# Optimization experiments

Measured on AMD Instinct MI355X. Metric: run time of the kernel, lower is better.

The kernel has to match this reference:

```python
import jax, jax.numpy as jnp
import numpy as np

ENC_IN = 512
D_MODEL = 1024
EMB_DIM = 32
IN_DIM = D_MODEL + EMB_DIM  # 1056
BATCH = 64


def setup_inputs() -> dict:
    key = jax.random.key(0)
    ks = jax.random.split(key, 12)
    s = 0.02
    return {
        "x": jax.random.normal(ks[0], (BATCH, ENC_IN, D_MODEL), dtype=jnp.float32),
        "emb": jax.random.normal(ks[1], (ENC_IN, EMB_DIM), dtype=jnp.float32) * s,
        # weights stored [in, out] (transposed vs torch Linear, same math)
        "w1": jax.random.normal(ks[2], (IN_DIM, IN_DIM), dtype=jnp.float32) * s,
        "b1": jnp.zeros((IN_DIM,), dtype=jnp.float32),
        "wq": jax.random.normal(ks[3], (IN_DIM, IN_DIM), dtype=jnp.float32) * s,
        "bq": jnp.zeros((IN_DIM,), dtype=jnp.float32),
        "wk": jax.random.normal(ks[4], (IN_DIM, IN_DIM), dtype=jnp.float32) * s,
        "bk": jnp.zeros((IN_DIM,), dtype=jnp.float32),
        "wv": jax.random.normal(ks[5], (IN_DIM, IN_DIM), dtype=jnp.float32) * s,
        "bv": jnp.zeros((IN_DIM,), dtype=jnp.float32),
        "w2": jax.random.normal(ks[6], (IN_DIM, D_MODEL), dtype=jnp.float32) * s,
        "b2": jnp.zeros((D_MODEL,), dtype=jnp.float32),
    }


def reference(x, emb, w1, b1, wq, bq, wk, bk, wv, bv, w2, b2):
    B = x.shape[0]
    # variable embedding: same for every batch element -> broadcast concat
    e = jnp.broadcast_to(emb[None, :, :], (B, ENC_IN, EMB_DIM))
    h = jnp.concatenate([x, e], axis=2)                      # [B, S, IN_DIM]
    h = jax.nn.leaky_relu(h @ w1 + b1, negative_slope=0.2)   # l1
    # hand-rolled self-attention: no scaling, softmax over last dim
    q = h @ wq + bq
    k = h @ wk + bk
    v = h @ wv + bv
    energy = jnp.einsum("bsd,btd->bst", q, k)                # [B, S, S]
    attn = jax.nn.softmax(energy, axis=-1)
    out = jnp.einsum("bst,btd->bsd", attn, v)                # [B, S, IN_DIM]
    return out @ w2 + b2                                     # [B, S, D_MODEL]
```

## Files before the change

### kernel.cpp

```cpp
#include <hip/hip_runtime.h>
#include <hip/hip_bf16.h>
#include <cstdint>

typedef __hip_bfloat16 bf16;
typedef __attribute__((ext_vector_type(8))) short short8;
typedef __attribute__((ext_vector_type(4))) float f32x4;

__device__ __forceinline__ void gload16(const bf16* g, bf16* l) {
    __builtin_amdgcn_global_load_lds(
        (__attribute__((address_space(1))) void*)g,
        (__attribute__((address_space(3))) void*)l, 16, 0, 0);
}
#define VMC(n) asm volatile("s_waitcnt vmcnt(" #n ")" ::: "memory")
__device__ __forceinline__ void bar() {
    asm volatile("" ::: "memory");
    __builtin_amdgcn_s_barrier();
    asm volatile("" ::: "memory");
}

__device__ __forceinline__ void stage_half(const bf16* __restrict__ G, int ld,
                                           int row0, int k0, bf16* lregion,
                                           int w, int lrow, int lslot)
{
    const bf16* s0 = G + (long long)(row0 + w * 8 + lrow) * ld + (k0 + lslot * 8);
    gload16(s0, lregion + (w * 64) * 8);
    gload16(s0 + (long long)64 * ld, lregion + (512 + w * 64) * 8);
}

#define LOAD_AI(dst, i_, mh, P) do { \
    _Pragma("unroll") for (int ks_ = 0; ks_ < 2; ++ks_) \
      dst[i_][ks_] = *(const short8*)((P) + ((mh) * 64 + (i_) * 16 + l15) * 64 \
                                         + (((ks_ * 4 + lq) ^ l7) * 8)); } while (0)
#define LOAD_B(nh, dst) do { _Pragma("unroll") for (int j_ = 0; j_ < 2; ++j_) { \
    _Pragma("unroll") for (int ks_ = 0; ks_ < 2; ++ks_) \
      dst[j_][ks_] = *(const short8*)(pb + (bhr + (nh) * 32 + j_ * 16 + l15) * 64 \
                                         + (((ks_ * 4 + lq) ^ l7) * 8)); } } while (0)
#define DO_Q(mh, nh, AF, BF) do { \
    __builtin_amdgcn_s_setprio(1); \
    _Pragma("unroll") for (int i_ = 0; i_ < 4; ++i_) \
      _Pragma("unroll") for (int j_ = 0; j_ < 2; ++j_) \
        _Pragma("unroll") for (int ks_ = 0; ks_ < 2; ++ks_) \
          acc[mh][nh][i_][j_] = __builtin_amdgcn_mfma_f32_16x16x32_bf16( \
              AF[i_][ks_], BF[j_][ks_], acc[mh][nh][i_][j_], 0, 0, 0); \
    __builtin_amdgcn_s_setprio(0); \
} while (0)

template<int OUT_BF16, int ACT, int BIASMODE, int ROUTE>
__global__ __launch_bounds__(512, 2)
void gemm256(const bf16* __restrict__ Abase, const bf16* __restrict__ Bbase,
             void* __restrict__ Cbase, const float* __restrict__ bias,
             int K, int lda, int ldb, int ldc, int nwrite,
             long long sA, long long sB, long long sC, long long segStride)
{
    __shared__ bf16 lds[2][2][2][8192];

    const int gx = gridDim.x, gy = gridDim.y;
    const int nwg = gx * gy * gridDim.z;
    const int lin = blockIdx.x + gx * (blockIdx.y + gy * blockIdx.z);
    const int qch = nwg >> 3, rch = nwg & 7;
    const int xcd = lin & 7, pos = lin >> 3;
    const int nl = (xcd < rch ? xcd * (qch + 1)
                              : rch * (qch + 1) + (xcd - rch) * qch) + pos;
    const int bz = nl / (gx * gy);
    const int rem = nl - bz * (gx * gy);
    const int by = rem / gx;
    const int bx = rem - by * gx;

    const int tid = threadIdx.x;
    const int wid = tid >> 6, lane = tid & 63;
    const int wm = wid >> 2, wn = wid & 3;
    const int l15 = lane & 15, l7 = lane & 7, lq = lane >> 4;
    const int lrow = lane >> 3, lslot = l7 ^ lrow;
    const int bhr = (wn & 1) * 64;

    const bf16* A = Abase + (long long)bz * sA;
    const bf16* B = Bbase + (long long)bz * sB;
    const int brow = by * 256, bcol = bx * 256;

    f32x4 acc[2][2][4][2] = {};
    short8 aFe[4][2], aFo[4][2], bF0[2][2], bF1[2][2];

    const int nt = K >> 6;

    stage_half(B, ldb, bcol,       0,  &lds[0][1][0][0], wid, lrow, lslot);
    stage_half(B, ldb, bcol + 128, 0,  &lds[0][1][1][0], wid, lrow, lslot);
    stage_half(A, lda, brow,       0,  &lds[0][0][0][0], wid, lrow, lslot);
    stage_half(A, lda, brow + 128, 0,  &lds[0][0][1][0], wid, lrow, lslot);
    stage_half(B, ldb, bcol,       64, &lds[1][1][0][0], wid, lrow, lslot);
    stage_half(B, ldb, bcol + 128, 64, &lds[1][1][1][0], wid, lrow, lslot);
    VMC(4);
    bar();

    for (int t = 0; t < nt; ++t) {
        const int b = t & 1;
        const bf16* pa = &lds[b][0][wm][0];
        const bf16* pb = &lds[b][1][wn >> 1][0];
        bf16* oA = &lds[b ^ 1][0][0][0];
        bf16* cB = &lds[b][1][0][0];
        const int t1 = (t + 1 == nt) ? 0 : t + 1;
        const int t2 = (t + 2 >= nt) ? t + 2 - nt : t + 2;
        const int k1 = t1 << 6, k2 = t2 << 6;

        LOAD_B(0, bF0);
        LOAD_AI(aFe, 0, 0, pa); LOAD_AI(aFe, 1, 0, pa);
        LOAD_AI(aFe, 2, 0, pa); LOAD_AI(aFe, 3, 0, pa);
        LOAD_B(1, bF1);
        stage_half(A, lda, brow, k1, oA, wid, lrow, lslot);
        bar();
        DO_Q(0, 0, aFe, bF0);
        bar();

        LOAD_AI(aFo, 0, 1, pa); LOAD_AI(aFo, 1, 1, pa);
        stage_half(A, lda, brow + 128, k1, oA + 8192, wid, lrow, lslot);
        bar();
        DO_Q(0, 1, aFe, bF1);
        bar();

        LOAD_AI(aFo, 2, 1, pa); LOAD_AI(aFo, 3, 1, pa);
        stage_half(B, ldb, bcol, k2, cB, wid, lrow, lslot);
        bar();
        DO_Q(1, 1, aFo, bF1);
        bar();

        stage_half(B, ldb, bcol + 128, k2, cB + 8192, wid, lrow, lslot);
        bar();
        DO_Q(1, 0, aFo, bF0);
        VMC(4);
        bar();
    }
    VMC(0);

    const long long cofs0 = (long long)bz * sC;
    #pragma unroll
    for (int mh = 0; mh < 2; ++mh)
      #pragma unroll
      for (int nh = 0; nh < 2; ++nh)
        #pragma unroll
        for (int i = 0; i < 4; ++i)
          #pragma unroll
          for (int j = 0; j < 2; ++j) {
              const int gc = bcol + wn * 64 + nh * 32 + j * 16 + l15;
              const bool wr = gc < nwrite;
              const int row0 = brow + wm * 128 + mh * 64 + i * 16 + lq * 4;
              if (wr) {
                  float bvv = 0.0f;
                  if (BIASMODE == 1) bvv = bias[gc];
                  if (BIASMODE == 3) bvv = bias[(long long)bz * 512 + gc];
                  if (ROUTE == 2 && gc < 1152) {
                      const int b_ = row0 >> 9, s_ = row0 & 511;
                      bf16 t4[4];
                      #pragma unroll
                      for (int rr = 0; rr < 4; ++rr) {
                          float vv = acc[mh][nh][i][j][rr] + bvv;
                          t4[rr] = (bf16)vv;
                      }
                      *(ushort4*)&((bf16*)Cbase)[((long long)b_ * 1280 + gc) * 512 + s_]
                          = *(ushort4*)t4;
                  } else {
                      long long base; int lc, ld;
                      if (ROUTE == 2) { base = segStride; lc = gc - 1152; ld = 1088; }
                      else { base = cofs0; lc = gc; ld = ldc; }
                      #pragma unroll
                      for (int rr = 0; rr < 4; ++rr) {
                          float vv = acc[mh][nh][i][j][rr] + bvv;
                          if (ACT) vv = vv > 0.0f ? vv : 0.2f * vv;
                          const long long cidx = base + (long long)(row0 + rr) * ld + lc;
                          if (OUT_BF16) ((bf16*)Cbase)[cidx] = (bf16)vv;
                          else          ((float*)Cbase)[cidx] = vv;
                      }
                  }
              }
          }
}

__global__ void concat_cast_kernel(const float* __restrict__ x,
                                   const float* __restrict__ emb,
                                   bf16* __restrict__ out)
{
    const int m = blockIdx.x;
    const int s = m & 511;
    const float* xr = x + (long long)m * 1024;
    bf16* orow = out + (long long)m * 1088;
    for (int g = threadIdx.x; g < 272; g += 256) {
        const int c = g * 4;
        float4 v;
        if (c < 1024)      v = *(const float4*)&xr[c];
        else if (c < 1056) v = *(const float4*)&emb[s * 32 + (c - 1024)];
        else               v = make_float4(0.f, 0.f, 0.f, 0.f);
        bf16 t[4] = { (bf16)v.x, (bf16)v.y, (bf16)v.z, (bf16)v.w };
        *(ushort4*)&orow[c] = *(ushort4*)t;
    }
}

__global__ void wprep_kernel(const float* __restrict__ w1, const float* __restrict__ wv,
                             const float* __restrict__ w2, const float* __restrict__ wq,
                             const float* __restrict__ wk,
                             bf16* __restrict__ w1T, bf16* __restrict__ Bqv,
                             bf16* __restrict__ w2T, bf16* __restrict__ wqC,
                             bf16* __restrict__ wkC)
{
    const int z = blockIdx.z;
    const int tx = threadIdx.x, ty = threadIdx.y;
    if (z >= 3) {
        const float* src = (z == 3) ? wq : wk;
        bf16* dst = (z == 3) ? wqC : wkC;
        const int r = blockIdx.y * 32 + ty, c = blockIdx.x * 32 + tx;
        if (r < 1280 && c < 1088) {
            float v = (r < 1056 && c < 1056) ? src[(long long)r * 1056 + c] : 0.0f;
            dst[(long long)r * 1088 + c] = (bf16)v;
        }
        return;
    }
    const float* src; bf16* dst; int NIN, NP, srcld;
    switch (z) {
        case 0: src = w1; dst = w1T; NIN = 1056; NP = 1280; srcld = 1056; break;
        case 1: src = wv; dst = Bqv; NIN = 1056; NP = 1152; srcld = 1056; break;
        default: src = w2; dst = w2T; NIN = 1024; NP = 1024; srcld = 1024; break;
    }
    const int KIN = 1056, KP = 1088;
    const int k0 = blockIdx.x * 32, n0 = blockIdx.y * 32;
    if (n0 >= NP) return;
    __shared__ float t[32][33];
    const int kk = k0 + ty, nn = n0 + tx;
    t[ty][tx] = (kk < KIN && nn < NIN) ? src[(long long)kk * srcld + nn] : 0.0f;
    __syncthreads();
    const int ko = k0 + tx, no = n0 + ty;
    if (no < NP && ko < KP)
        dst[(long long)no * KP + ko] = (bf16)t[tx][ty];
}

__global__ void vtzero_kernel(bf16* __restrict__ vt)
{
    const long long i = ((long long)blockIdx.x * 256 + threadIdx.x) * 8;
    const int per_batch = 128 * 512;
    const int b = (int)(i / per_batch);
    const long long r = i - (long long)b * per_batch;
    ushort4 z4 = make_ushort4(0, 0, 0, 0);
    bf16* p = &vt[(long long)b * (1280LL * 512) + 1152LL * 512 + r];
    *(ushort4*)p = z4;
    *(ushort4*)(p + 4) = z4;
}

__global__ void uvec_kernel(const float* __restrict__ wk, const float* __restrict__ bq,
                            float* __restrict__ u)
{
    const int wid = threadIdx.x >> 6, lane = threadIdx.x & 63;
    const int e = blockIdx.x * 4 + wid;
    if (e >= 1088) return;
    float s = 0.0f;
    if (e < 1056) {
        for (int d = lane; d < 1056; d += 64)
            s += wk[(long long)e * 1056 + d] * bq[d];
    }
    #pragma unroll
    for (int sh = 32; sh > 0; sh >>= 1) s += __shfl_xor(s, sh);
    if (lane == 0) u[e] = s;
}

__global__ __launch_bounds__(256)
void cvec_kernel(const bf16* __restrict__ h, const float* __restrict__ u,
                 float* __restrict__ c)
{
    const int wid = threadIdx.x >> 6, lane = threadIdx.x & 63;
    const long long row = (long long)blockIdx.x * 4 + wid;
    const bf16* hr = h + row * 1088;
    float s = 0.0f;
    #pragma unroll
    for (int j = 0; j < 17; ++j)
        s += (float)hr[j * 64 + lane] * u[j * 64 + lane];
    #pragma unroll
    for (int sh = 32; sh > 0; sh >>= 1) s += __shfl_xor(s, sh);
    if (lane == 0) c[row] = s;
}

__global__ void biasprep_kernel(const float* __restrict__ b1, const float* __restrict__ bv,
                                const float* __restrict__ b2,
                                float* __restrict__ b1p, float* __restrict__ bqv2,
                                float* __restrict__ b2p)
{
    const int i = blockIdx.x * 256 + threadIdx.x;
    if (i < 1088) {
        b1p[i] = (i < 1056) ? b1[i] : 0.0f;
    } else if (i < 1088 + 2304) {
        const int j = i - 1088;
        bqv2[j] = (j < 1056) ? bv[j] : 0.0f;
    } else if (i < 1088 + 2304 + 1024) {
        b2p[i - (1088 + 2304)] = b2[i - (1088 + 2304)];
    }
}

__global__ __launch_bounds__(256)
void softmax_kernel(const float* __restrict__ e, bf16* __restrict__ p)
{
    const int wid = threadIdx.x >> 6, lane = threadIdx.x & 63;
    const long long row = (long long)blockIdx.x * 4 + wid;
    const float* er = e + row * 512;
    float v[8];
    float mx = -3.0e38f;
    #pragma unroll
    for (int j = 0; j < 8; ++j) { v[j] = er[j * 64 + lane]; mx = fmaxf(mx, v[j]); }
    #pragma unroll
    for (int s = 32; s > 0; s >>= 1) mx = fmaxf(mx, __shfl_xor(mx, s));
    float sum = 0.0f;
    #pragma unroll
    for (int j = 0; j < 8; ++j) { v[j] = __expf(v[j] - mx); sum += v[j]; }
    #pragma unroll
    for (int s = 32; s > 0; s >>= 1) sum += __shfl_xor(sum, s);
    const float inv = 1.0f / sum;
    bf16* pr = p + row * 512;
    #pragma unroll
    for (int j = 0; j < 8; ++j) pr[j * 64 + lane] = (bf16)(v[j] * inv);
}

extern "C" void kernel_launch(void* const* d_in, const int* in_sizes, int n_in,
                              void* d_out, int out_size, void* d_ws, size_t ws_size,
                              hipStream_t stream)
{
    const float* x   = (const float*)d_in[0];
    const float* emb = (const float*)d_in[1];
    const float* w1  = (const float*)d_in[2];
    const float* b1  = (const float*)d_in[3];
    const float* wq  = (const float*)d_in[4];
    const float* bq  = (const float*)d_in[5];
    const float* wk  = (const float*)d_in[6];
    const float* wv  = (const float*)d_in[8];
    const float* bv  = (const float*)d_in[9];
    const float* w2  = (const float*)d_in[10];
    const float* b2  = (const float*)d_in[11];
    float* out = (float*)d_out;

    const long long Mrows = 32768;
    const int KR = 1088;

    char* ws = (char*)d_ws;
    size_t off = 0;
    auto alloc = [&](size_t bytes) -> char* {
        char* p = ws + off;
        off += (bytes + 255) & ~(size_t)255;
        return p;
    };
    char* R1   = alloc((size_t)Mrows * KR * 2);
    char* Rh   = alloc((size_t)Mrows * KR * 2);
    char* Rq   = alloc((size_t)Mrows * KR * 2);
    bf16* vT   = (bf16*)alloc((size_t)64 * 1280 * 512 * 2);
    bf16* w1T  = (bf16*)alloc((size_t)1280 * KR * 2);
    bf16* Bqv  = (bf16*)alloc((size_t)2432 * KR * 2);
    bf16* w2T  = (bf16*)alloc((size_t)1024 * KR * 2);
    bf16* wqC  = (bf16*)alloc((size_t)1280 * KR * 2);
    bf16* wkC  = (bf16*)alloc((size_t)1280 * KR * 2);
    float* b1p  = (float*)alloc((size_t)1088 * 4);
    float* bqv2 = (float*)alloc((size_t)2304 * 4);
    float* b2p  = (float*)alloc((size_t)1024 * 4);
    float* uvec = (float*)alloc((size_t)1088 * 4);
    float* cvec = (float*)alloc((size_t)Mrows * 4);

    bf16*  hcat   = (bf16*)R1;
    float* energy = (float*)R1;
    bf16*  pv     = (bf16*)R1;
    bf16*  h      = (bf16*)Rh;
    bf16*  qbuf   = (bf16*)Rq;
    bf16*  attn   = (bf16*)Rq;

    concat_cast_kernel<<<32768, 256, 0, stream>>>(x, emb, hcat);
    wprep_kernel<<<dim3(34, 40, 5), dim3(32, 32), 0, stream>>>(
        w1, wv, w2, wq, wk, w1T, Bqv, w2T, wqC, wkC);
    uvec_kernel<<<272, 256, 0, stream>>>(wk, bq, uvec);
    biasprep_kernel<<<18, 256, 0, stream>>>(b1, bv, b2, b1p, bqv2, b2p);
    vtzero_kernel<<<2048, 256, 0, stream>>>(vT);

    gemm256<1, 0, 0, 0><<<dim3(5, 5, 1), 512, 0, stream>>>(
        wkC, wqC, Bqv + 1152LL * KR, nullptr,
        KR, KR, KR, KR, KR, 0, 0, 0, 0);
    gemm256<1, 1, 1, 0><<<dim3(5, 128, 1), 512, 0, stream>>>(
        hcat, w1T, h, b1p, KR, KR, KR, KR, KR, 0, 0, 0, 0);
    cvec_kernel<<<8192, 256, 0, stream>>>(h, uvec, cvec);
    gemm256<1, 0, 1, 2><<<dim3(9, 128, 1), 512, 0, stream>>>(
        h, Bqv, vT, bqv2, KR, KR, KR, 0, 2240, 0, 0, 0,
        (long long)(qbuf - vT));
    gemm256<0, 0, 3, 0><<<dim3(2, 2, 64), 512, 0, stream>>>(
        qbuf, h, energy, cvec, KR, KR, KR, 512, 512,
        512LL * KR, 512LL * KR, 512LL * 512, 0);
    softmax_kernel<<<8192, 256, 0, stream>>>(energy, attn);
    gemm256<1, 0, 0, 0><<<dim3(5, 2, 64), 512, 0, stream>>>(
        attn, vT, pv, nullptr, 512, 512, 512, KR, KR,
        512LL * 512, 1280LL * 512, 512LL * KR, 0);
    gemm256<0, 0, 1, 0><<<dim3(4, 128, 1), 512, 0, stream>>>(
        pv, w2T, out, b2p, KR, KR, KR, 1024, 1024, 0, 0, 0, 0);
}
```

Measured before the change: 600.7 us.

## Fold w2 into value projection to drop final output GEMM

Precomputes Wv·W2 as a combined weight (plus bv·W2 + b2 as a bias) so the V projection directly produces a 1024-wide v2 in transposed layout, and attention-times-v2 writes the final output. This removes the separate pv buffer and the final full-size projection GEMM, and also the vT padding-zero kernel. The cost is an extra small weight-product GEMM and a serial bias kernel, and a change in bf16 rounding order because the products are fused into one weight.

```diff
diff --git a/kernel.cpp b/kernel.cpp
--- a/kernel.cpp
+++ b/kernel.cpp
@@ -146,7 +146,7 @@
                   float bvv = 0.0f;
                   if (BIASMODE == 1) bvv = bias[gc];
                   if (BIASMODE == 3) bvv = bias[(long long)bz * 512 + gc];
-                  if (ROUTE == 2 && gc < 1152) {
+                  if (ROUTE == 2 && gc < 1024) {
                       const int b_ = row0 >> 9, s_ = row0 & 511;
                       bf16 t4[4];
                       #pragma unroll
@@ -154,11 +154,11 @@
                           float vv = acc[mh][nh][i][j][rr] + bvv;
                           t4[rr] = (bf16)vv;
                       }
-                      *(ushort4*)&((bf16*)Cbase)[((long long)b_ * 1280 + gc) * 512 + s_]
+                      *(ushort4*)&((bf16*)Cbase)[((long long)b_ * 1024 + gc) * 512 + s_]
                           = *(ushort4*)t4;
                   } else {
                       long long base; int lc, ld;
-                      if (ROUTE == 2) { base = segStride; lc = gc - 1152; ld = 1088; }
+                      if (ROUTE == 2) { base = segStride; lc = gc - 1024; ld = 1088; }
                       else { base = cofs0; lc = gc; ld = ldc; }
                       #pragma unroll
                       for (int rr = 0; rr < 4; ++rr) {
@@ -195,15 +195,15 @@
 __global__ void wprep_kernel(const float* __restrict__ w1, const float* __restrict__ wv,
                              const float* __restrict__ w2, const float* __restrict__ wq,
                              const float* __restrict__ wk,
-                             bf16* __restrict__ w1T, bf16* __restrict__ Bqv,
+                             bf16* __restrict__ w1T, bf16* __restrict__ wvC,
                              bf16* __restrict__ w2T, bf16* __restrict__ wqC,
                              bf16* __restrict__ wkC)
 {
     const int z = blockIdx.z;
     const int tx = threadIdx.x, ty = threadIdx.y;
-    if (z >= 3) {
-        const float* src = (z == 3) ? wq : wk;
-        bf16* dst = (z == 3) ? wqC : wkC;
+    if (z == 1 || z >= 3) {
+        const float* src = (z == 1) ? wv : (z == 3) ? wq : wk;
+        bf16* dst = (z == 1) ? wvC : (z == 3) ? wqC : wkC;
         const int r = blockIdx.y * 32 + ty, c = blockIdx.x * 32 + tx;
         if (r < 1280 && c < 1088) {
             float v = (r < 1056 && c < 1056) ? src[(long long)r * 1056 + c] : 0.0f;
@@ -212,11 +212,8 @@
         return;
     }
     const float* src; bf16* dst; int NIN, NP, srcld;
-    switch (z) {
-        case 0: src = w1; dst = w1T; NIN = 1056; NP = 1280; srcld = 1056; break;
-        case 1: src = wv; dst = Bqv; NIN = 1056; NP = 1152; srcld = 1056; break;
-        default: src = w2; dst = w2T; NIN = 1024; NP = 1024; srcld = 1024; break;
-    }
+    if (z == 0) { src = w1; dst = w1T; NIN = 1056; NP = 1280; srcld = 1056; }
+    else        { src = w2; dst = w2T; NIN = 1024; NP = 1024; srcld = 1024; }
     const int KIN = 1056, KP = 1088;
     const int k0 = blockIdx.x * 32, n0 = blockIdx.y * 32;
     if (n0 >= NP) return;
@@ -229,18 +226,6 @@
         dst[(long long)no * KP + ko] = (bf16)t[tx][ty];
 }
 
-__global__ void vtzero_kernel(bf16* __restrict__ vt)
-{
-    const long long i = ((long long)blockIdx.x * 256 + threadIdx.x) * 8;
-    const int per_batch = 128 * 512;
-    const int b = (int)(i / per_batch);
-    const long long r = i - (long long)b * per_batch;
-    ushort4 z4 = make_ushort4(0, 0, 0, 0);
-    bf16* p = &vt[(long long)b * (1280LL * 512) + 1152LL * 512 + r];
-    *(ushort4*)p = z4;
-    *(ushort4*)(p + 4) = z4;
-}
-
 __global__ void uvec_kernel(const float* __restrict__ wk, const float* __restrict__ bq,
                             float* __restrict__ u)
 {
@@ -273,20 +258,20 @@
     if (lane == 0) c[row] = s;
 }
 
-__global__ void biasprep_kernel(const float* __restrict__ b1, const float* __restrict__ bv,
-                                const float* __restrict__ b2,
-                                float* __restrict__ b1p, float* __restrict__ bqv2,
-                                float* __restrict__ b2p)
+__global__ void bvw2_kernel(const float* __restrict__ bv, const float* __restrict__ w2,
+                            const float* __restrict__ b2, float* __restrict__ b2p2)
+{
+    const int n = blockIdx.x * 256 + threadIdx.x;
+    float s = b2[n];
+    for (int o = 0; o < 1056; ++o)
+        s += bv[o] * w2[(long long)o * 1024 + n];
+    b2p2[n] = s;
+}
+
+__global__ void biasprep_kernel(const float* __restrict__ b1, float* __restrict__ b1p)
 {
     const int i = blockIdx.x * 256 + threadIdx.x;
-    if (i < 1088) {
-        b1p[i] = (i < 1056) ? b1[i] : 0.0f;
-    } else if (i < 1088 + 2304) {
-        const int j = i - 1088;
-        bqv2[j] = (j < 1056) ? bv[j] : 0.0f;
-    } else if (i < 1088 + 2304 + 1024) {
-        b2p[i - (1088 + 2304)] = b2[i - (1088 + 2304)];
-    }
+    if (i < 1088) b1p[i] = (i < 1056) ? b1[i] : 0.0f;
 }
 
 __global__ __launch_bounds__(256)
@@ -342,48 +327,48 @@
     char* R1   = alloc((size_t)Mrows * KR * 2);
     char* Rh   = alloc((size_t)Mrows * KR * 2);
     char* Rq   = alloc((size_t)Mrows * KR * 2);
-    bf16* vT   = (bf16*)alloc((size_t)64 * 1280 * 512 * 2);
+    bf16* v2T  = (bf16*)alloc((size_t)64 * 1024 * 512 * 2);
     bf16* w1T  = (bf16*)alloc((size_t)1280 * KR * 2);
-    bf16* Bqv  = (bf16*)alloc((size_t)2432 * KR * 2);
+    bf16* Bqv  = (bf16*)alloc((size_t)2304 * KR * 2);
     bf16* w2T  = (bf16*)alloc((size_t)1024 * KR * 2);
     bf16* wqC  = (bf16*)alloc((size_t)1280 * KR * 2);
     bf16* wkC  = (bf16*)alloc((size_t)1280 * KR * 2);
+    bf16* wvC  = (bf16*)alloc((size_t)1280 * KR * 2);
     float* b1p  = (float*)alloc((size_t)1088 * 4);
-    float* bqv2 = (float*)alloc((size_t)2304 * 4);
-    float* b2p  = (float*)alloc((size_t)1024 * 4);
+    float* b2p2 = (float*)alloc((size_t)1024 * 4);
     float* uvec = (float*)alloc((size_t)1088 * 4);
     float* cvec = (float*)alloc((size_t)Mrows * 4);
 
     bf16*  hcat   = (bf16*)R1;
     float* energy = (float*)R1;
-    bf16*  pv     = (bf16*)R1;
     bf16*  h      = (bf16*)Rh;
     bf16*  qbuf   = (bf16*)Rq;
     bf16*  attn   = (bf16*)Rq;
 
     concat_cast_kernel<<<32768, 256, 0, stream>>>(x, emb, hcat);
     wprep_kernel<<<dim3(34, 40, 5), dim3(32, 32), 0, stream>>>(
-        w1, wv, w2, wq, wk, w1T, Bqv, w2T, wqC, wkC);
+        w1, wv, w2, wq, wk, w1T, wvC, w2T, wqC, wkC);
     uvec_kernel<<<272, 256, 0, stream>>>(wk, bq, uvec);
-    biasprep_kernel<<<18, 256, 0, stream>>>(b1, bv, b2, b1p, bqv2, b2p);
-    vtzero_kernel<<<2048, 256, 0, stream>>>(vT);
+    biasprep_kernel<<<5, 256, 0, stream>>>(b1, b1p);
+    bvw2_kernel<<<4, 256, 0, stream>>>(bv, w2, b2, b2p2);
 
     gemm256<1, 0, 0, 0><<<dim3(5, 5, 1), 512, 0, stream>>>(
-        wkC, wqC, Bqv + 1152LL * KR, nullptr,
+        wkC, wqC, Bqv + 1024LL * KR, nullptr,
+        KR, KR, KR, KR, KR, 0, 0, 0, 0);
+    gemm256<1, 0, 0, 0><<<dim3(5, 4, 1), 512, 0, stream>>>(
+        w2T, wvC, Bqv, nullptr,
         KR, KR, KR, KR, KR, 0, 0, 0, 0);
     gemm256<1, 1, 1, 0><<<dim3(5, 128, 1), 512, 0, stream>>>(
         hcat, w1T, h, b1p, KR, KR, KR, KR, KR, 0, 0, 0, 0);
     cvec_kernel<<<8192, 256, 0, stream>>>(h, uvec, cvec);
-    gemm256<1, 0, 1, 2><<<dim3(9, 128, 1), 512, 0, stream>>>(
-        h, Bqv, vT, bqv2, KR, KR, KR, 0, 2240, 0, 0, 0,
-        (long long)(qbuf - vT));
+    gemm256<1, 0, 0, 2><<<dim3(9, 128, 1), 512, 0, stream>>>(
+        h, Bqv, v2T, nullptr, KR, KR, KR, 0, 2112, 0, 0, 0,
+        (long long)(qbuf - v2T));
     gemm256<0, 0, 3, 0><<<dim3(2, 2, 64), 512, 0, stream>>>(
         qbuf, h, energy, cvec, KR, KR, KR, 512, 512,
         512LL * KR, 512LL * KR, 512LL * 512, 0);
     softmax_kernel<<<8192, 256, 0, stream>>>(energy, attn);
-    gemm256<1, 0, 0, 0><<<dim3(5, 2, 64), 512, 0, stream>>>(
-        attn, vT, pv, nullptr, 512, 512, 512, KR, KR,
-        512LL * 512, 1280LL * 512, 512LL * KR, 0);
-    gemm256<0, 0, 1, 0><<<dim3(4, 128, 1), 512, 0, stream>>>(
-        pv, w2T, out, b2p, KR, KR, KR, 1024, 1024, 0, 0, 0, 0);
-}
+    gemm256<0, 0, 1, 0><<<dim3(4, 2, 64), 512, 0, stream>>>(
+        attn, v2T, out, b2p2, 512, 512, 512, 1024, 1024,
+        512LL * 512, 1024LL * 512, 512LL * 1024, 0);
+}
```

Result: faster. 579.1 us (-3.6%).
